# Performance work log

Hardware: AMD Instinct MI355X
Metric: run time of the kernel (lower is better)

The kernel has to match this reference:

```python
import jax, jax.numpy as jnp
import numpy as np

B, S, H, E, K, DFF = 4, 2048, 1024, 8, 2, 4096


def setup_inputs() -> dict:
    key = jax.random.key(0)
    k0, k1, k2, k3 = jax.random.split(key, 4)
    sc = 0.02
    return {
        "x": jax.random.normal(k0, (B, S, H), jnp.float32),
        "gate_W": jax.random.normal(k1, (H, E), jnp.float32) * sc,
        "gate_b": jnp.zeros((E,), jnp.float32),
        "W1": jax.random.normal(k2, (H, DFF), jnp.float32) * sc,
        "b1": jnp.zeros((DFF,), jnp.float32),
        "W2": jax.random.normal(k3, (DFF, H), jnp.float32) * sc,
        "b2": jnp.zeros((H,), jnp.float32),
    }


def reference(x, gate_W, gate_b, W1, b1, W2, b2):
    b, s, h = x.shape
    x_flat = x.reshape(-1, h)                      # [T, H]
    gate_scores = x_flat @ gate_W + gate_b         # [T, E]
    top_k_scores, top_k_idx = jax.lax.top_k(gate_scores, K)   # [T, K]
    top_k_w = jax.nn.softmax(top_k_scores, axis=-1)           # [T, K]

    # All experts share the same weights (ModuleList reuses one module), so
    # sum_i w_i * expert_i(x) == expert(x) * sum_i w_i. top_k indices are
    # unique per token, so the per-token combine weight is sum of top-k weights.
    hdd = jax.nn.gelu(x_flat @ W1 + b1, approximate=False)    # [T, DFF]
    y = hdd @ W2 + b2                                         # [T, H]
    tok_w = top_k_w.sum(axis=-1)                              # [T] (== 1.0)
    output = (y * tok_w[:, None]).reshape(b, s, h)

    expert_load = gate_scores.mean(axis=0)                    # [E]
    aux_loss = (expert_load ** 2).sum()
    exp_counts = jnp.zeros((E,), jnp.int32).at[top_k_idx.ravel()].add(1)
    return output, aux_loss, exp_counts
```

## Files before the change

kernel.cpp:

```cpp
#include <hip/hip_runtime.h>
#include <hip/hip_bf16.h>
#include <math.h>

#define Tn   8192
#define Hn   1024
#define En   8
#define DFFn 4096

typedef __attribute__((ext_vector_type(8))) short bf16x8;
typedef __attribute__((ext_vector_type(4))) float f32x4;

static __device__ inline unsigned short f2bf(float f) {
    __hip_bfloat16 h = __float2bfloat16(f);
    return __builtin_bit_cast(unsigned short, h);
}

__global__ __launch_bounds__(256) void prep(
    const float* __restrict__ W1, const float* __restrict__ W2,
    __hip_bfloat16* __restrict__ W1t, __hip_bfloat16* __restrict__ W2t,
    const float* __restrict__ x, const float* __restrict__ gW,
    const float* __restrict__ gb, unsigned short* __restrict__ xbf,
    float* __restrict__ tokw, float* __restrict__ load_sum,
    int* __restrict__ counts)
{
    const int tid = threadIdx.x;
    int id = blockIdx.x;

    if (id < 8192) {
        __shared__ float tile[32][33];
        const float* src; __hip_bfloat16* dst; int Kd, Nd, bx, by;
        if (id < 4096) { src = W1; dst = W1t; Kd = Hn;   Nd = DFFn;
                         bx = id & 127; by = id >> 7; }
        else { id -= 4096; src = W2; dst = W2t; Kd = DFFn; Nd = Hn;
               bx = id & 31;  by = id >> 5; }
        const int n0 = bx * 32, k0 = by * 32;
        const int tx = tid & 31, ty = tid >> 5;
        #pragma unroll
        for (int r = 0; r < 32; r += 8)
            tile[ty + r][tx] = src[(size_t)(k0 + ty + r) * Nd + n0 + tx];
        __syncthreads();
        #pragma unroll
        for (int r = 0; r < 32; r += 8)
            dst[(size_t)(n0 + ty + r) * Kd + k0 + tx] =
                __float2bfloat16(tile[tx][ty + r]);
        return;
    }

    __shared__ float s_load[En];
    __shared__ int   s_cnt[En];
    if (tid < En) { s_load[tid] = 0.f; s_cnt[tid] = 0; }
    __syncthreads();

    const int bid  = id - 8192;
    const int lane = tid & 63;
    const int wv   = tid >> 6;

    for (int tok = bid * 4 + wv; tok < Tn; tok += 2048) {
        const float4* xr = (const float4*)(x + (size_t)tok * Hn);
        float acc[8] = {0.f,0.f,0.f,0.f,0.f,0.f,0.f,0.f};
        #pragma unroll
        for (int j = 0; j < Hn / 256; ++j) {
            int h4 = j * 64 + lane;
            float4 xv = xr[h4];
            ushort4 pk;
            pk.x = f2bf(xv.x); pk.y = f2bf(xv.y);
            pk.z = f2bf(xv.z); pk.w = f2bf(xv.w);
            ((ushort4*)xbf)[(size_t)tok * (Hn / 4) + h4] = pk;
            const float* wr = gW + (size_t)h4 * 4 * En;
            float xs[4] = {xv.x, xv.y, xv.z, xv.w};
            #pragma unroll
            for (int c = 0; c < 4; ++c)
                #pragma unroll
                for (int e = 0; e < 8; ++e)
                    acc[e] += xs[c] * wr[c * 8 + e];
        }
        #pragma unroll
        for (int e = 0; e < 8; ++e) {
            float v = acc[e];
            #pragma unroll
            for (int off = 32; off > 0; off >>= 1) v += __shfl_xor(v, off, 64);
            acc[e] = v + gb[e];
        }
        if (lane == 0) {
            #pragma unroll
            for (int e = 0; e < 8; ++e) atomicAdd(&s_load[e], acc[e]);
            int i1 = 0; float v1 = acc[0];
            #pragma unroll
            for (int e = 1; e < 8; ++e) if (acc[e] > v1) { v1 = acc[e]; i1 = e; }
            int i2 = -1; float v2 = -3.0e38f;
            #pragma unroll
            for (int e = 0; e < 8; ++e) if (e != i1 && acc[e] > v2) { v2 = acc[e]; i2 = e; }
            atomicAdd(&s_cnt[i1], 1);
            atomicAdd(&s_cnt[i2], 1);
            float e2 = __expf(v2 - v1);
            float t  = 1.0f + e2;
            tokw[tok] = 1.0f / t + e2 / t;
        }
    }
    __syncthreads();
    if (tid < En) {
        atomicAdd(&load_sum[tid], s_load[tid]);
        atomicAdd(&counts[tid],   s_cnt[tid]);
    }
}

template<int EPI>
__global__ __launch_bounds__(256) void gemm_bt(
    const __hip_bfloat16* __restrict__ A,
    const __hip_bfloat16* __restrict__ Bt,
    const float* __restrict__ bias,
    const float* __restrict__ tokw,
    void* __restrict__ C, int N, int K, int nxlog2,
    const float* __restrict__ load_sum, const int* __restrict__ counts,
    float* __restrict__ out_tail)
{
    __shared__ __hip_bfloat16 sA[128 * 32];
    __shared__ __hip_bfloat16 sB[128 * 32];

    const int tid  = threadIdx.x;
    const int lane = tid & 63;
    const int wv   = tid >> 6;
    const int wm   = (wv >> 1) * 64;
    const int wn   = (wv & 1) * 64;

    const int id     = blockIdx.x;
    const int xcd    = id & 7;
    const int slot   = id >> 3;
    const int bx     = slot & ((1 << nxlog2) - 1);
    const int ylocal = slot >> nxlog2;
    const int y_per  = (int)((gridDim.x >> 3) >> nxlog2);
    const int by     = xcd * y_per + ylocal;

    const int m0 = by * 128, n0 = bx * 128;

    f32x4 acc[4][4];
    const f32x4 zero = {0.f, 0.f, 0.f, 0.f};
    #pragma unroll
    for (int i = 0; i < 4; ++i)
        #pragma unroll
        for (int j = 0; j < 4; ++j) acc[i][j] = zero;

    const int r0 = tid >> 2;
    const int kc = (((tid & 3) - (r0 >> 1)) & 3) * 8;
    const __hip_bfloat16* gA = A  + (size_t)(m0 + r0) * K + kc;
    const __hip_bfloat16* gB = Bt + (size_t)(n0 + r0) * K + kc;
    const size_t half = (size_t)64 * K;

    const int fr = lane & 15;
    const int fs = (((lane >> 4) + (fr >> 1)) & 3) * 8;

    for (int k0 = 0; k0 < K; k0 += 32) {
        __syncthreads();
        __builtin_amdgcn_global_load_lds(
            (const __attribute__((address_space(1))) void*)(gA + k0),
            (__attribute__((address_space(3))) void*)(sA + tid * 8), 16, 0, 0);
        __builtin_amdgcn_global_load_lds(
            (const __attribute__((address_space(1))) void*)(gA + half + k0),
            (__attribute__((address_space(3))) void*)(sA + 2048 + tid * 8), 16, 0, 0);
        __builtin_amdgcn_global_load_lds(
            (const __attribute__((address_space(1))) void*)(gB + k0),
            (__attribute__((address_space(3))) void*)(sB + tid * 8), 16, 0, 0);
        __builtin_amdgcn_global_load_lds(
            (const __attribute__((address_space(1))) void*)(gB + half + k0),
            (__attribute__((address_space(3))) void*)(sB + 2048 + tid * 8), 16, 0, 0);
        __syncthreads();

        bf16x8 af[4], bfr[4];
        #pragma unroll
        for (int mi = 0; mi < 4; ++mi)
            af[mi] = *(const bf16x8*)(sA + (wm + mi * 16 + fr) * 32 + fs);
        #pragma unroll
        for (int ni = 0; ni < 4; ++ni)
            bfr[ni] = *(const bf16x8*)(sB + (wn + ni * 16 + fr) * 32 + fs);
        #pragma unroll
        for (int mi = 0; mi < 4; ++mi)
            #pragma unroll
            for (int ni = 0; ni < 4; ++ni)
                acc[mi][ni] = __builtin_amdgcn_mfma_f32_16x16x32_bf16(
                    af[mi], bfr[ni], acc[mi][ni], 0, 0, 0);
    }

    #pragma unroll
    for (int mi = 0; mi < 4; ++mi) {
        #pragma unroll
        for (int ni = 0; ni < 4; ++ni) {
            const int col   = n0 + wn + ni * 16 + (lane & 15);
            const int rbase = m0 + wm + mi * 16 + (lane >> 4) * 4;
            const float bv  = bias[col];
            #pragma unroll
            for (int i = 0; i < 4; ++i) {
                const int row = rbase + i;
                float v = acc[mi][ni][i] + bv;
                if (EPI == 0) {
                    float vv = v * v;
                    float z  = v * __fmaf_rn(vv, -0.07135607f, -1.59576912f);
                    float e  = __expf(z);
                    float g  = v * __builtin_amdgcn_rcpf(1.0f + e);
                    ((__hip_bfloat16*)C)[(size_t)row * N + col] = __float2bfloat16(g);
                } else {
                    ((float*)C)[(size_t)row * N + col] = v * tokw[row];
                }
            }
        }
    }

    if (EPI == 0 && id == (int)gridDim.x - 1 && tid == 0) {
        float aux = 0.f;
        #pragma unroll
        for (int e = 0; e < En; ++e) {
            float m = load_sum[e] * (1.0f / (float)Tn);
            aux += m * m;
        }
        out_tail[0] = aux;
        #pragma unroll
        for (int e = 0; e < En; ++e) out_tail[1 + e] = (float)counts[e];
    }
}

extern "C" void kernel_launch(void* const* d_in, const int* in_sizes, int n_in,
                              void* d_out, int out_size, void* d_ws, size_t ws_size,
                              hipStream_t stream)
{
    const float* x  = (const float*)d_in[0];
    const float* gW = (const float*)d_in[1];
    const float* gb = (const float*)d_in[2];
    const float* W1 = (const float*)d_in[3];
    const float* b1 = (const float*)d_in[4];
    const float* W2 = (const float*)d_in[5];
    const float* b2 = (const float*)d_in[6];
    float* out = (float*)d_out;

    char* ws = (char*)d_ws;
    __hip_bfloat16* xbf = (__hip_bfloat16*)ws;  ws += (size_t)Tn * Hn * 2;
    __hip_bfloat16* W1t = (__hip_bfloat16*)ws;  ws += (size_t)Hn * DFFn * 2;
    __hip_bfloat16* W2t = (__hip_bfloat16*)ws;  ws += (size_t)Hn * DFFn * 2;
    __hip_bfloat16* hdd = (__hip_bfloat16*)ws;  ws += (size_t)Tn * DFFn * 2;
    float* tokw     = (float*)ws;               ws += (size_t)Tn * 4;
    float* load_sum = (float*)ws;               ws += En * 4;
    int*   counts   = (int*)ws;                 ws += En * 4;

    hipMemsetAsync(load_sum, 0, En * 4 * 2, stream);

    prep<<<8704, 256, 0, stream>>>(W1, W2, W1t, W2t, x, gW, gb,
                                   (unsigned short*)xbf, tokw, load_sum, counts);

    gemm_bt<0><<<(DFFn / 128) * (Tn / 128), 256, 0, stream>>>(
        xbf, W1t, b1, nullptr, hdd, DFFn, Hn, 5,
        load_sum, counts, out + (size_t)Tn * Hn);
    gemm_bt<1><<<(Hn / 128) * (Tn / 128), 256, 0, stream>>>(
        hdd, W2t, b2, tokw, out, Hn, DFFn, 3,
        nullptr, nullptr, nullptr);
}
```

Measured before the change: 324.2 us.

## Overlap W2 transpose with first GEMM and vectorize weight transposes

The W2 fp32-to-bf16 transpose moves out of the prep kernel into extra tail blocks of the first GEMM launch, so it can overlap GEMM1 work, and the aux-loss/count output moves there too. Both transposes now use float4 loads and ushort4 stores through a padded shared tile, replacing scalar accesses. The gating GEMV stages gate_W into shared memory in an expert-major layout, so each lane reads float4 weights instead of scattered global loads. The cost is extra shared memory in prep (about 32KB), which may lower its occupancy, and GEMM1's grid now mixes in non-GEMM blocks.

```diff
diff --git a/kernel.cpp b/kernel.cpp
--- a/kernel.cpp
+++ b/kernel.cpp
@@ -16,42 +16,48 @@
 }
 
 __global__ __launch_bounds__(256) void prep(
-    const float* __restrict__ W1, const float* __restrict__ W2,
-    __hip_bfloat16* __restrict__ W1t, __hip_bfloat16* __restrict__ W2t,
+    const float* __restrict__ W1, unsigned short* __restrict__ W1t,
     const float* __restrict__ x, const float* __restrict__ gW,
     const float* __restrict__ gb, unsigned short* __restrict__ xbf,
     float* __restrict__ tokw, float* __restrict__ load_sum,
     int* __restrict__ counts)
 {
+    __shared__ float smem[8 * 1024 + En];
+    __shared__ int   s_cnt[En];
     const int tid = threadIdx.x;
-    int id = blockIdx.x;
-
-    if (id < 8192) {
-        __shared__ float tile[32][33];
-        const float* src; __hip_bfloat16* dst; int Kd, Nd, bx, by;
-        if (id < 4096) { src = W1; dst = W1t; Kd = Hn;   Nd = DFFn;
-                         bx = id & 127; by = id >> 7; }
-        else { id -= 4096; src = W2; dst = W2t; Kd = DFFn; Nd = Hn;
-               bx = id & 31;  by = id >> 5; }
+    const int id  = blockIdx.x;
+
+    if (id < 4096) {
+        float* tile = smem;
+        const int bx = id & 127, by = id >> 7;
         const int n0 = bx * 32, k0 = by * 32;
-        const int tx = tid & 31, ty = tid >> 5;
-        #pragma unroll
-        for (int r = 0; r < 32; r += 8)
-            tile[ty + r][tx] = src[(size_t)(k0 + ty + r) * Nd + n0 + tx];
-        __syncthreads();
-        #pragma unroll
-        for (int r = 0; r < 32; r += 8)
-            dst[(size_t)(n0 + ty + r) * Kd + k0 + tx] =
-                __float2bfloat16(tile[tx][ty + r]);
+        const int r  = tid >> 3, c4 = (tid & 7) * 4;
+        float4 v = *(const float4*)(W1 + (size_t)(k0 + r) * DFFn + n0 + c4);
+        tile[(c4 + 0) * 33 + r] = v.x;
+        tile[(c4 + 1) * 33 + r] = v.y;
+        tile[(c4 + 2) * 33 + r] = v.z;
+        tile[(c4 + 3) * 33 + r] = v.w;
+        __syncthreads();
+        ushort4 pk;
+        pk.x = f2bf(tile[r * 33 + c4 + 0]);
+        pk.y = f2bf(tile[r * 33 + c4 + 1]);
+        pk.z = f2bf(tile[r * 33 + c4 + 2]);
+        pk.w = f2bf(tile[r * 33 + c4 + 3]);
+        *(ushort4*)(W1t + (size_t)(n0 + r) * Hn + k0 + c4) = pk;
         return;
     }
 
-    __shared__ float s_load[En];
-    __shared__ int   s_cnt[En];
+    float* gwt    = smem;
+    float* s_load = smem + 8 * 1024;
     if (tid < En) { s_load[tid] = 0.f; s_cnt[tid] = 0; }
+    #pragma unroll
+    for (int i = 0; i < 32; ++i) {
+        int f = tid + i * 256;
+        gwt[(f & 7) * 1024 + (f >> 3)] = gW[f];
+    }
     __syncthreads();
 
-    const int bid  = id - 8192;
+    const int bid  = id - 4096;
     const int lane = tid & 63;
     const int wv   = tid >> 6;
 
@@ -66,13 +72,11 @@
             pk.x = f2bf(xv.x); pk.y = f2bf(xv.y);
             pk.z = f2bf(xv.z); pk.w = f2bf(xv.w);
             ((ushort4*)xbf)[(size_t)tok * (Hn / 4) + h4] = pk;
-            const float* wr = gW + (size_t)h4 * 4 * En;
-            float xs[4] = {xv.x, xv.y, xv.z, xv.w};
-            #pragma unroll
-            for (int c = 0; c < 4; ++c)
-                #pragma unroll
-                for (int e = 0; e < 8; ++e)
-                    acc[e] += xs[c] * wr[c * 8 + e];
+            #pragma unroll
+            for (int e = 0; e < 8; ++e) {
+                const float4 w = *(const float4*)(gwt + e * 1024 + h4 * 4);
+                acc[e] += xv.x * w.x + xv.y * w.y + xv.z * w.z + xv.w * w.w;
+            }
         }
         #pragma unroll
         for (int e = 0; e < 8; ++e) {
@@ -110,25 +114,59 @@
     const __hip_bfloat16* __restrict__ Bt,
     const float* __restrict__ bias,
     const float* __restrict__ tokw,
-    void* __restrict__ C, int N, int K, int nxlog2,
+    void* __restrict__ C, int N, int K, int nxlog2, int nblk,
+    const float* __restrict__ W2, unsigned short* __restrict__ W2t,
     const float* __restrict__ load_sum, const int* __restrict__ counts,
     float* __restrict__ out_tail)
 {
     __shared__ __hip_bfloat16 sA[128 * 32];
     __shared__ __hip_bfloat16 sB[128 * 32];
 
-    const int tid  = threadIdx.x;
+    const int tid = threadIdx.x;
+    const int id  = blockIdx.x;
+
+    if (EPI == 0 && id >= nblk) {
+        const int tb = id - nblk;
+        float* tile = (float*)sA;
+        const int bx = tb & 31, by = tb >> 5;
+        const int n0 = bx * 32, k0 = by * 32;
+        const int r  = tid >> 3, c4 = (tid & 7) * 4;
+        float4 v = *(const float4*)(W2 + (size_t)(k0 + r) * Hn + n0 + c4);
+        tile[(c4 + 0) * 33 + r] = v.x;
+        tile[(c4 + 1) * 33 + r] = v.y;
+        tile[(c4 + 2) * 33 + r] = v.z;
+        tile[(c4 + 3) * 33 + r] = v.w;
+        __syncthreads();
+        ushort4 pk;
+        pk.x = f2bf(tile[r * 33 + c4 + 0]);
+        pk.y = f2bf(tile[r * 33 + c4 + 1]);
+        pk.z = f2bf(tile[r * 33 + c4 + 2]);
+        pk.w = f2bf(tile[r * 33 + c4 + 3]);
+        *(ushort4*)(W2t + (size_t)(n0 + r) * DFFn + k0 + c4) = pk;
+        if (tb == 0 && tid == 0) {
+            float aux = 0.f;
+            #pragma unroll
+            for (int e = 0; e < En; ++e) {
+                float m = load_sum[e] * (1.0f / (float)Tn);
+                aux += m * m;
+            }
+            out_tail[0] = aux;
+            #pragma unroll
+            for (int e = 0; e < En; ++e) out_tail[1 + e] = (float)counts[e];
+        }
+        return;
+    }
+
     const int lane = tid & 63;
     const int wv   = tid >> 6;
     const int wm   = (wv >> 1) * 64;
     const int wn   = (wv & 1) * 64;
 
-    const int id     = blockIdx.x;
     const int xcd    = id & 7;
     const int slot   = id >> 3;
     const int bx     = slot & ((1 << nxlog2) - 1);
     const int ylocal = slot >> nxlog2;
-    const int y_per  = (int)((gridDim.x >> 3) >> nxlog2);
+    const int y_per  = (nblk >> 3) >> nxlog2;
     const int by     = xcd * y_per + ylocal;
 
     const int m0 = by * 128, n0 = bx * 128;
@@ -203,18 +241,6 @@
             }
         }
     }
-
-    if (EPI == 0 && id == (int)gridDim.x - 1 && tid == 0) {
-        float aux = 0.f;
-        #pragma unroll
-        for (int e = 0; e < En; ++e) {
-            float m = load_sum[e] * (1.0f / (float)Tn);
-            aux += m * m;
-        }
-        out_tail[0] = aux;
-        #pragma unroll
-        for (int e = 0; e < En; ++e) out_tail[1 + e] = (float)counts[e];
-    }
 }
 
 extern "C" void kernel_launch(void* const* d_in, const int* in_sizes, int n_in,
@@ -241,13 +267,13 @@
 
     hipMemsetAsync(load_sum, 0, En * 4 * 2, stream);
 
-    prep<<<8704, 256, 0, stream>>>(W1, W2, W1t, W2t, x, gW, gb,
+    prep<<<4608, 256, 0, stream>>>(W1, (unsigned short*)W1t, x, gW, gb,
                                    (unsigned short*)xbf, tokw, load_sum, counts);
 
-    gemm_bt<0><<<(DFFn / 128) * (Tn / 128), 256, 0, stream>>>(
-        xbf, W1t, b1, nullptr, hdd, DFFn, Hn, 5,
-        load_sum, counts, out + (size_t)Tn * Hn);
-    gemm_bt<1><<<(Hn / 128) * (Tn / 128), 256, 0, stream>>>(
-        hdd, W2t, b2, tokw, out, Hn, DFFn, 3,
-        nullptr, nullptr, nullptr);
-}
+    gemm_bt<0><<<2048 + 4096, 256, 0, stream>>>(
+        xbf, W1t, b1, nullptr, hdd, DFFn, Hn, 5, 2048,
+        W2, (unsigned short*)W2t, load_sum, counts, out + (size_t)Tn * Hn);
+    gemm_bt<1><<<512, 256, 0, stream>>>(
+        hdd, W2t, b2, tokw, out, Hn, DFFn, 3, 512,
+        nullptr, nullptr, nullptr, nullptr, nullptr);
+}
```

Result: no change. 323.2 us (-0.3%).
